# Optimization experiments

Measured on AMD Instinct MI355X. Metric: run time of the kernel, lower is better.

The kernel has to match this reference:

```python
import jax, jax.numpy as jnp
import numpy as np

N = 512
L = 1.0
DX = L / (N - 1)
DT = 1e-07
NUM_STEPS = 200
MB = 256  # material_boundary[1]


def setup_inputs() -> dict:
    key = jax.random.key(0)
    u0 = jax.random.normal(key, (N, N), dtype=jnp.float32)
    one = jnp.ones((1,), dtype=jnp.float32)
    return {"u0": u0, "k1": one, "k2": one, "alpha1": one, "alpha2": one}


def reference(u0, k1, k2, alpha1, alpha2):
    k1 = k1.reshape(())
    k2 = k2.reshape(())
    alpha1 = alpha1.reshape(())
    alpha2 = alpha2.reshape(())
    col_is_left = (jnp.arange(N) < MB)  # columns [:MB] get material 1
    material_map = jnp.broadcast_to(jnp.where(col_is_left, alpha1, alpha2), (N, N))
    k_map = jnp.broadcast_to(jnp.where(col_is_left, k1, k2), (N, N))
    alpha = material_map[1:-1, 1:-1]
    kappa = k_map[1:-1, 1:-1]
    dx2 = DX * DX
    ii = MB - 1  # interface column index
    k_left = k_map[:, ii]
    k_right = k_map[:, ii + 1]

    def step(T, _):
        Tc = T[1:-1, 1:-1]
        T_xx = (T[:-2, 1:-1] - 2.0 * Tc + T[2:, 1:-1]) / dx2
        T_yy = (T[1:-1, :-2] - 2.0 * Tc + T[1:-1, 2:]) / dx2
        T_x = (T[2:, 1:-1] - T[:-2, 1:-1]) / (2.0 * DX)
        T_y = (T[1:-1, 2:] - T[1:-1, :-2]) / (2.0 * DX)
        Tn_int = (Tc
                  - DT * (Tc ** 2 * T_x - Tc * T_y) * kappa
                  + DT * alpha * (T_xx + T_yy)
                  + DT * kappa * (Tc ** 3 - Tc ** 2 + Tc))
        Tn = T.at[1:-1, 1:-1].set(Tn_int)
        # material interface condition (uses old T values, as in source)
        Tn = Tn.at[:, ii].set((k_left * T[:, ii + 1] + k_right * T[:, ii - 1]) / (k_left + k_right))
        # Neumann-like boundary copies, in the same order as the source
        Tn = Tn.at[0, :].set(Tn[1, :])
        Tn = Tn.at[-1, :].set(Tn[-2, :])
        Tn = Tn.at[:, 0].set(Tn[:, 1])
        Tn = Tn.at[:, -1].set(Tn[:, -2])
        return Tn, Tn

    # torch code records T before each of num_steps iterations and returns [1:],
    # i.e. the states after steps 1..num_steps-1
    _, ys = jax.lax.scan(step, u0, None, length=NUM_STEPS - 1)
    return ys  # (NUM_STEPS-1, N, N)
```

## Files before the change

kernel.cpp:

```cpp
#include <hip/hip_runtime.h>

#define GN 512
#define GNN (GN * GN)
#define NSTEPS 199

#define TS 32
#define KS 16
#define HS 64
#define WROWS 8
#define NW 8
#define BTH 512

__constant__ const float kCdiff = (float)(1e-7 * 511.0 * 511.0);
__constant__ const float kCadv  = (float)(1e-7 * 511.0 / 2.0);
__constant__ const float kCrea  = 1e-7f;

__global__ __launch_bounds__(BTH) void adr_fused(
    const float* __restrict__ src, float* __restrict__ dstbase, int nsteps,
    const float* __restrict__ pk1, const float* __restrict__ pk2,
    const float* __restrict__ pa1, const float* __restrict__ pa2)
{
    __shared__ float xg[2][2][NW][HS];

    const int lane = threadIdx.x & 63;
    const int w    = threadIdx.x >> 6;
    const int bx = blockIdx.x & 15;
    const int by = blockIdx.x >> 4;
    const int r0 = by * TS;
    const int c0 = bx * TS;
    const int rb = r0 - KS;
    const int cb = c0 - KS;
    const int gc  = cb + lane;
    const int gr0 = rb + w * WROWS;

    const float k1 = pk1[0];
    const float k2 = pk2[0];
    const float a1 = pa1[0];
    const float a2 = pa2[0];

    const float kap = (gc < 256) ? k1 : k2;
    const float alp = (gc < 256) ? a1 : a2;
    const bool  ifc = (gc == 255);
    const float inv12 = 1.0f / (k1 + k2);
    const float ckA = kap * kCadv;
    const float ckD = alp * kCdiff;
    const float ckR = kCrea * kap;

    const int srcL = (lane == 0) ? 0 : lane - 1;
    const int srcR = (lane == HS - 1) ? HS - 1 : lane + 1;

    float cur[WROWS];
    const int gcc = min(max(gc, 0), GN - 1);
    #pragma unroll
    for (int k = 0; k < WROWS; ++k) {
        const int gr = min(max(gr0 + k, 0), GN - 1);
        cur[k] = src[gr * GN + gcc];
    }

    const bool fixTop = (by == 0)  && (w == 2);
    const bool fixBot = (by == 15) && (w == 5);
    const bool fixL   = (bx == 0);
    const bool fixR   = (bx == 15);
    const bool stores = (w >= 2 && w <= 5) && (lane >= 16 && lane < 48);

    int par = 0;
    for (int s = 0; s < nsteps; ++s) {
        xg[par][0][w][lane] = cur[0];
        xg[par][1][w][lane] = cur[WROWS - 1];
        __syncthreads();
        const float above = (w > 0)      ? xg[par][1][w - 1][lane] : cur[0];
        const float below = (w < NW - 1) ? xg[par][0][w + 1][lane] : cur[WROWS - 1];

        float nxt[WROWS];
        #pragma unroll
        for (int k = 0; k < WROWS; ++k) {
            const float tc = cur[k];
            const float tm = (k == 0)         ? above : cur[k - 1];
            const float tp = (k == WROWS - 1) ? below : cur[k + 1];
            const float tl = __shfl(tc, srcL);
            const float tr = __shfl(tc, srcR);
            const float adv = ckA * (tc * tc * (tp - tm) - tc * (tr - tl));
            const float dif = ckD * ((tm + tp + tl + tr) - 4.0f * tc);
            const float rea = ckR * ((tc * tc * tc - tc * tc) + tc);
            float v = tc - adv + dif + rea;
            const float vif = (k1 * tr + k2 * tl) * inv12;
            nxt[k] = ifc ? vif : v;
        }

        if (fixTop) nxt[0] = nxt[1];
        if (fixBot) nxt[WROWS - 1] = nxt[WROWS - 2];
        if (fixL) {
            #pragma unroll
            for (int k = 0; k < WROWS; ++k) {
                const float t = __shfl(nxt[k], 17);
                if (lane <= 16) nxt[k] = t;
            }
        }
        if (fixR) {
            #pragma unroll
            for (int k = 0; k < WROWS; ++k) {
                const float t = __shfl(nxt[k], 46);
                if (lane >= 47) nxt[k] = t;
            }
        }

        float* __restrict__ dst = dstbase + (size_t)s * GNN;
        if (stores) {
            #pragma unroll
            for (int k = 0; k < WROWS; ++k)
                dst[(gr0 + k) * GN + gc] = nxt[k];
        }

        #pragma unroll
        for (int k = 0; k < WROWS; ++k) cur[k] = nxt[k];
        par ^= 1;
    }
}

extern "C" void kernel_launch(void* const* d_in, const int* in_sizes, int n_in,
                              void* d_out, int out_size, void* d_ws, size_t ws_size,
                              hipStream_t stream) {
    (void)in_sizes; (void)n_in; (void)out_size; (void)d_ws; (void)ws_size;

    const float* u0 = (const float*)d_in[0];
    const float* k1 = (const float*)d_in[1];
    const float* k2 = (const float*)d_in[2];
    const float* a1 = (const float*)d_in[3];
    const float* a2 = (const float*)d_in[4];
    float* out = (float*)d_out;

    const dim3 block(BTH);
    const dim3 grid((GN / TS) * (GN / TS));

    const float* src = u0;
    int step = 0;
    while (step < NSTEPS) {
        const int ns = (NSTEPS - step < KS) ? (NSTEPS - step) : KS;
        float* dstbase = out + (size_t)step * GNN;
        adr_fused<<<grid, block, 0, stream>>>(src, dstbase, ns, k1, k2, a1, a2);
        src = dstbase + (size_t)(ns - 1) * GNN;
        step += ns;
    }
}
```

Baseline: 407.6 us.

## Use single-wave 2D register tiles with shuffle-only halo exchange

Replaces the 512-thread block (8 waves exchanging row halos through shared memory with a barrier every step) with one 64-lane wave per block. Each lane holds a 4x4 register tile, the wave covers a 32x32 haloed region that yields a 16x16 output tile, and neighbours are exchanged only through wave shuffles. Loads and stores become float4 vectors, and interface and boundary handling is applied only in blocks that need it. The cost is a larger halo fraction (16x16 output from 32x32 compute), fewer fused steps per launch (8 instead of 16, so more launches), and a grid of 1024 small blocks.

After: 391.8 us. -3.9%, faster.

```diff
diff --git a/kernel.cpp b/kernel.cpp
--- a/kernel.cpp
+++ b/kernel.cpp
@@ -4,116 +4,145 @@
 #define GNN (GN * GN)
 #define NSTEPS 199
 
-#define TS 32
-#define KS 16
-#define HS 64
-#define WROWS 8
-#define NW 8
-#define BTH 512
+#define TS 16
+#define KS 8
+#define HS 32
+#define PR 4
+#define PC 4
 
 __constant__ const float kCdiff = (float)(1e-7 * 511.0 * 511.0);
 __constant__ const float kCadv  = (float)(1e-7 * 511.0 / 2.0);
 __constant__ const float kCrea  = 1e-7f;
 
-__global__ __launch_bounds__(BTH) void adr_fused(
+__global__ __launch_bounds__(64) void adr_fused(
     const float* __restrict__ src, float* __restrict__ dstbase, int nsteps,
     const float* __restrict__ pk1, const float* __restrict__ pk2,
     const float* __restrict__ pa1, const float* __restrict__ pa2)
 {
-    __shared__ float xg[2][2][NW][HS];
-
     const int lane = threadIdx.x & 63;
-    const int w    = threadIdx.x >> 6;
-    const int bx = blockIdx.x & 15;
-    const int by = blockIdx.x >> 4;
-    const int r0 = by * TS;
-    const int c0 = bx * TS;
-    const int rb = r0 - KS;
-    const int cb = c0 - KS;
-    const int gc  = cb + lane;
-    const int gr0 = rb + w * WROWS;
+    const int cg = lane & 7;
+    const int rg = lane >> 3;
+    const int bx = blockIdx.x & 31;
+    const int by = blockIdx.x >> 5;
+    const int rb = by * TS - KS;
+    const int cb = bx * TS - KS;
+    const int pr0 = rb + rg * PR;
+    const int pc0 = cb + cg * PC;
 
     const float k1 = pk1[0];
     const float k2 = pk2[0];
     const float a1 = pa1[0];
     const float a2 = pa2[0];
+    const float inv12 = 1.0f / (k1 + k2);
 
-    const float kap = (gc < 256) ? k1 : k2;
-    const float alp = (gc < 256) ? a1 : a2;
-    const bool  ifc = (gc == 255);
-    const float inv12 = 1.0f / (k1 + k2);
-    const float ckA = kap * kCadv;
-    const float ckD = alp * kCdiff;
-    const float ckR = kCrea * kap;
-
-    const int srcL = (lane == 0) ? 0 : lane - 1;
-    const int srcR = (lane == HS - 1) ? HS - 1 : lane + 1;
-
-    float cur[WROWS];
-    const int gcc = min(max(gc, 0), GN - 1);
+    float ckA[PC], ckD[PC], ckR[PC];
     #pragma unroll
-    for (int k = 0; k < WROWS; ++k) {
-        const int gr = min(max(gr0 + k, 0), GN - 1);
-        cur[k] = src[gr * GN + gcc];
+    for (int c = 0; c < PC; ++c) {
+        const int gc = pc0 + c;
+        const float kap = (gc < 256) ? k1 : k2;
+        const float alp = (gc < 256) ? a1 : a2;
+        ckA[c] = kap * kCadv;
+        ckD[c] = alp * kCdiff;
+        ckR[c] = kCrea * kap;
     }
 
-    const bool fixTop = (by == 0)  && (w == 2);
-    const bool fixBot = (by == 15) && (w == 5);
-    const bool fixL   = (bx == 0);
-    const bool fixR   = (bx == 15);
-    const bool stores = (w >= 2 && w <= 5) && (lane >= 16 && lane < 48);
+    const int laneL = (lane + 63) & 63;
+    const int laneR = (lane + 1) & 63;
+    const int laneU = (lane + 56) & 63;
+    const int laneD = (lane + 8) & 63;
 
-    int par = 0;
-    for (int s = 0; s < nsteps; ++s) {
-        xg[par][0][w][lane] = cur[0];
-        xg[par][1][w][lane] = cur[WROWS - 1];
-        __syncthreads();
-        const float above = (w > 0)      ? xg[par][1][w - 1][lane] : cur[0];
-        const float below = (w < NW - 1) ? xg[par][0][w + 1][lane] : cur[WROWS - 1];
+    const bool interior = (bx > 0 && bx < 31 && by > 0 && by < 31);
+    const bool hasIface = (bx == 15 || bx == 16);
+    const bool fTop = (by == 0), fBot = (by == 31);
+    const bool fL = (bx == 0), fR = (bx == 31);
+    const bool storeLane = (rg >= 2 && rg <= 5 && cg >= 2 && cg <= 5);
 
-        float nxt[WROWS];
+    float cur[PR][PC];
+    if (interior) {
         #pragma unroll
-        for (int k = 0; k < WROWS; ++k) {
-            const float tc = cur[k];
-            const float tm = (k == 0)         ? above : cur[k - 1];
-            const float tp = (k == WROWS - 1) ? below : cur[k + 1];
-            const float tl = __shfl(tc, srcL);
-            const float tr = __shfl(tc, srcR);
-            const float adv = ckA * (tc * tc * (tp - tm) - tc * (tr - tl));
-            const float dif = ckD * ((tm + tp + tl + tr) - 4.0f * tc);
-            const float rea = ckR * ((tc * tc * tc - tc * tc) + tc);
-            float v = tc - adv + dif + rea;
-            const float vif = (k1 * tr + k2 * tl) * inv12;
-            nxt[k] = ifc ? vif : v;
+        for (int r = 0; r < PR; ++r) {
+            const float4 v = *reinterpret_cast<const float4*>(
+                src + (pr0 + r) * GN + pc0);
+            cur[r][0] = v.x; cur[r][1] = v.y; cur[r][2] = v.z; cur[r][3] = v.w;
         }
-
-        if (fixTop) nxt[0] = nxt[1];
-        if (fixBot) nxt[WROWS - 1] = nxt[WROWS - 2];
-        if (fixL) {
+    } else {
+        #pragma unroll
+        for (int r = 0; r < PR; ++r) {
+            const int gr = min(max(pr0 + r, 0), GN - 1);
             #pragma unroll
-            for (int k = 0; k < WROWS; ++k) {
-                const float t = __shfl(nxt[k], 17);
-                if (lane <= 16) nxt[k] = t;
+            for (int c = 0; c < PC; ++c) {
+                const int gc = min(max(pc0 + c, 0), GN - 1);
+                cur[r][c] = src[gr * GN + gc];
             }
         }
-        if (fixR) {
+    }
+
+    for (int s = 0; s < nsteps; ++s) {
+        float tlE[PR], trE[PR], tmE[PC], tpE[PC];
+        #pragma unroll
+        for (int r = 0; r < PR; ++r) tlE[r] = __shfl(cur[r][PC - 1], laneL);
+        #pragma unroll
+        for (int r = 0; r < PR; ++r) trE[r] = __shfl(cur[r][0], laneR);
+        #pragma unroll
+        for (int c = 0; c < PC; ++c) tmE[c] = __shfl(cur[PR - 1][c], laneU);
+        #pragma unroll
+        for (int c = 0; c < PC; ++c) tpE[c] = __shfl(cur[0][c], laneD);
+
+        float nxt[PR][PC];
+        #pragma unroll
+        for (int r = 0; r < PR; ++r) {
             #pragma unroll
-            for (int k = 0; k < WROWS; ++k) {
-                const float t = __shfl(nxt[k], 46);
-                if (lane >= 47) nxt[k] = t;
+            for (int c = 0; c < PC; ++c) {
+                const float tc = cur[r][c];
+                const float tm = (r > 0)      ? cur[r - 1][c] : tmE[c];
+                const float tp = (r < PR - 1) ? cur[r + 1][c] : tpE[c];
+                const float tl = (c > 0)      ? cur[r][c - 1] : tlE[r];
+                const float tr = (c < PC - 1) ? cur[r][c + 1] : trE[r];
+                const float t2 = tc * tc;
+                const float adv = ckA[c] * (t2 * (tp - tm) - tc * (tr - tl));
+                const float dif = ckD[c] * ((tm + tp + tl + tr) - 4.0f * tc);
+                const float rea = ckR[c] * ((t2 * tc - t2) + tc);
+                float v = tc - adv + dif + rea;
+                if (hasIface) {
+                    const float vif = (k1 * tr + k2 * tl) * inv12;
+                    v = (pc0 + c == 255) ? vif : v;
+                }
+                nxt[r][c] = v;
             }
         }
 
+        if (fTop && rg == 2) {
+            #pragma unroll
+            for (int c = 0; c < PC; ++c) nxt[0][c] = nxt[1][c];
+        }
+        if (fBot && rg == 5) {
+            #pragma unroll
+            for (int c = 0; c < PC; ++c) nxt[3][c] = nxt[2][c];
+        }
+        if (fL && cg == 2) {
+            #pragma unroll
+            for (int r = 0; r < PR; ++r) nxt[r][0] = nxt[r][1];
+        }
+        if (fR && cg == 5) {
+            #pragma unroll
+            for (int r = 0; r < PR; ++r) nxt[r][3] = nxt[r][2];
+        }
+
         float* __restrict__ dst = dstbase + (size_t)s * GNN;
-        if (stores) {
+        if (storeLane) {
             #pragma unroll
-            for (int k = 0; k < WROWS; ++k)
-                dst[(gr0 + k) * GN + gc] = nxt[k];
+            for (int r = 0; r < PR; ++r) {
+                float4 v;
+                v.x = nxt[r][0]; v.y = nxt[r][1];
+                v.z = nxt[r][2]; v.w = nxt[r][3];
+                *reinterpret_cast<float4*>(dst + (pr0 + r) * GN + pc0) = v;
+            }
         }
 
         #pragma unroll
-        for (int k = 0; k < WROWS; ++k) cur[k] = nxt[k];
-        par ^= 1;
+        for (int r = 0; r < PR; ++r)
+            #pragma unroll
+            for (int c = 0; c < PC; ++c) cur[r][c] = nxt[r][c];
     }
 }
 
@@ -129,7 +158,7 @@
     const float* a2 = (const float*)d_in[4];
     float* out = (float*)d_out;
 
-    const dim3 block(BTH);
+    const dim3 block(64);
     const dim3 grid((GN / TS) * (GN / TS));
 
     const float* src = u0;
```
